# Optimization experiments

Hardware: AMD Instinct MI355X
Metric: run time of the kernel (lower is better)

## Reference

```python
import jax, jax.numpy as jnp
import numpy as np

B, N, D = 16384, 30, 128  # batch, max_neighbors, model_dim


def setup_inputs() -> dict:
    key = jax.random.key(0)
    k1, k2, k3, k4, k5 = jax.random.split(key, 5)
    rel_embeds = jax.random.normal(k1, (B, N, D), dtype=jnp.float32)
    ent_embeds = jax.random.normal(k2, (B, N, D), dtype=jnp.float32)
    mask = jax.random.randint(k3, (B, N), 0, 2).astype(jnp.bool_)  # True = masked
    # neigh_att_W: Linear(2D -> D), xavier-normal weight; neigh_att_u: Linear(D -> 1)
    std_w = float(np.sqrt(2.0 / (2 * D + D)))
    W_w = jax.random.normal(k4, (D, 2 * D), dtype=jnp.float32) * std_w
    b_w = jnp.zeros((D,), dtype=jnp.float32)
    std_u = float(np.sqrt(2.0 / (D + 1)))
    W_u = jax.random.normal(k5, (1, D), dtype=jnp.float32) * std_u
    b_u = jnp.zeros((1,), dtype=jnp.float32)
    return {"rel_embeds": rel_embeds, "ent_embeds": ent_embeds, "mask": mask,
            "W_w": W_w, "b_w": b_w, "W_u": W_u, "b_u": b_u}


def reference(rel_embeds, ent_embeds, mask, W_w, b_w, W_u, b_u):
    # concat along feature dim -> [B, N, 2D]
    concat = jnp.concatenate([rel_embeds, ent_embeds], axis=-1)
    h = jnp.tanh(jnp.einsum('bnf,df->bnd', concat, W_w) + b_w)      # [B, N, D]
    att = jnp.einsum('bnd,od->bno', h, W_u) + b_u                   # [B, N, 1]
    att = jnp.where(mask[..., None], -jnp.inf, att)
    att = jax.nn.softmax(att, axis=1)[..., 0]                       # [B, N]
    out = jnp.einsum('bn,bnd->bd', att, ent_embeds)                 # [B, D]
    return jnp.tanh(out)
```

## Files before the change

### kernel.cpp

```cpp
#include <hip/hip_runtime.h>
#include <cstdint>
#include <cstddef>


#define WAVES 4
#define BLOCK 256
#define NPAD 32
#define LDS_STRIDE 264

typedef __attribute__((ext_vector_type(8))) short short8;
typedef __attribute__((ext_vector_type(4))) float f32x4;

__device__ __forceinline__ float fast_tanh(float x) {
  float e = __expf(2.0f * x);
  return 1.0f - 2.0f / (e + 1.0f);
}

__device__ __forceinline__ void cvt_hilo(float f, unsigned short& h, unsigned short& l) {
  unsigned int bits = __float_as_uint(f);
  h = (unsigned short)(bits >> 16);
  float r = f - __uint_as_float(bits & 0xFFFF0000u);
  l = (unsigned short)(__float_as_uint(r) >> 16);
}

__global__ __launch_bounds__(BLOCK, 2) void hetrognn_kernel(
    const float* __restrict__ rel, const float* __restrict__ ent,
    const int* __restrict__ mask, const float* __restrict__ Ww,
    const float* __restrict__ bw, const float* __restrict__ Wu,
    const float* __restrict__ bu, float* __restrict__ out, int Btot) {
  __shared__ unsigned short Ahi[NPAD * LDS_STRIDE];
  __shared__ unsigned short Alo[NPAD * LDS_STRIDE];
  __shared__ float pscore[WAVES][NPAD];
  __shared__ float att[NPAD];

  const int tid = threadIdx.x;
  const int wave = tid >> 6;
  const int lane = tid & 63;
  const int l15 = lane & 15;
  const int quad = lane >> 4;

  short8 whi[2][8], wlo[2][8];
  float bwv[2], uv[2];
#pragma unroll
  for (int c = 0; c < 2; ++c) {
    const int d = wave * 32 + c * 16 + l15;
    bwv[c] = bw[d];
    uv[c] = Wu[d];
#pragma unroll
    for (int ks = 0; ks < 8; ++ks) {
      const float* wp = Ww + d * 256 + ks * 32 + quad * 8;
#pragma unroll
      for (int j = 0; j < 8; ++j) {
        unsigned short h, l;
        cvt_hilo(wp[j], h, l);
        whi[c][ks][j] = (short)h;
        wlo[c][ks][j] = (short)l;
      }
    }
  }
  const float buv = bu[0];

  for (int b = blockIdx.x; b < Btot; b += gridDim.x) {
    const float* rel_b = rel + (size_t)b * 3840;
    const float* ent_b = ent + (size_t)b * 3840;

#pragma unroll
    for (int it = 0; it < 8; ++it) {
      const int i4 = tid + it * 256;
      const int row = i4 >> 6;
      const int k4 = (i4 & 63) << 2;
      float4 v = make_float4(0.f, 0.f, 0.f, 0.f);
      if (row < 30) {
        const float* src = (k4 < 128) ? (rel_b + row * 128 + k4)
                                      : (ent_b + row * 128 + (k4 - 128));
        v = *(const float4*)src;
      }
      unsigned short h0, h1, h2, h3, l0, l1, l2, l3;
      cvt_hilo(v.x, h0, l0);
      cvt_hilo(v.y, h1, l1);
      cvt_hilo(v.z, h2, l2);
      cvt_hilo(v.w, h3, l3);
      uint2 hh, ll;
      hh.x = (unsigned int)h0 | ((unsigned int)h1 << 16);
      hh.y = (unsigned int)h2 | ((unsigned int)h3 << 16);
      ll.x = (unsigned int)l0 | ((unsigned int)l1 << 16);
      ll.y = (unsigned int)l2 | ((unsigned int)l3 << 16);
      *(uint2*)&Ahi[row * LDS_STRIDE + k4] = hh;
      *(uint2*)&Alo[row * LDS_STRIDE + k4] = ll;
    }
    __syncthreads();

#pragma unroll
    for (int mt = 0; mt < 2; ++mt) {
      f32x4 acc0 = {0.f, 0.f, 0.f, 0.f};
      f32x4 acc1 = {0.f, 0.f, 0.f, 0.f};
      const int arow = mt * 16 + l15;
      const unsigned short* abase = &Ahi[arow * LDS_STRIDE + quad * 8];
      const unsigned short* lbase = &Alo[arow * LDS_STRIDE + quad * 8];
#pragma unroll
      for (int ks = 0; ks < 8; ++ks) {
        short8 ah = *(const short8*)(abase + ks * 32);
        short8 al = *(const short8*)(lbase + ks * 32);
        acc0 = __builtin_amdgcn_mfma_f32_16x16x32_bf16(ah, whi[0][ks], acc0, 0, 0, 0);
        acc1 = __builtin_amdgcn_mfma_f32_16x16x32_bf16(ah, whi[1][ks], acc1, 0, 0, 0);
        acc0 = __builtin_amdgcn_mfma_f32_16x16x32_bf16(al, whi[0][ks], acc0, 0, 0, 0);
        acc1 = __builtin_amdgcn_mfma_f32_16x16x32_bf16(al, whi[1][ks], acc1, 0, 0, 0);
        acc0 = __builtin_amdgcn_mfma_f32_16x16x32_bf16(ah, wlo[0][ks], acc0, 0, 0, 0);
        acc1 = __builtin_amdgcn_mfma_f32_16x16x32_bf16(ah, wlo[1][ks], acc1, 0, 0, 0);
      }
      float part[4];
#pragma unroll
      for (int reg = 0; reg < 4; ++reg) {
        float h0 = fast_tanh(acc0[reg] + bwv[0]);
        float h1 = fast_tanh(acc1[reg] + bwv[1]);
        part[reg] = uv[0] * h0 + uv[1] * h1;
      }
#pragma unroll
      for (int m = 1; m < 16; m <<= 1) {
#pragma unroll
        for (int reg = 0; reg < 4; ++reg) part[reg] += __shfl_xor(part[reg], m, 64);
      }
      float v = (l15 == 0) ? part[0] : (l15 == 1) ? part[1] : (l15 == 2) ? part[2] : part[3];
      if (l15 < 4) pscore[wave][mt * 16 + quad * 4 + l15] = v;
    }
    __syncthreads();

    if (tid < 32) {
      const int n = tid;
      float raw = pscore[0][n] + pscore[1][n] + pscore[2][n] + pscore[3][n] + buv;
      const bool valid = (n < 30) && (mask[(size_t)b * 30 + n] == 0);
      float sc = valid ? raw : -INFINITY;
      float mx = sc;
#pragma unroll
      for (int m = 1; m < 32; m <<= 1) mx = fmaxf(mx, __shfl_xor(mx, m, 64));
      float e = valid ? __expf(sc - mx) : 0.f;
      float sm = e;
#pragma unroll
      for (int m = 1; m < 32; m <<= 1) sm += __shfl_xor(sm, m, 64);
      att[n] = e / sm;
    }
    __syncthreads();

    if (tid < 128) {
      const int d = tid;
      const float* ep = ent_b + d;
      float acc = 0.f;
#pragma unroll
      for (int n = 0; n < 30; ++n) acc += att[n] * ep[n * 128];
      out[(size_t)b * 128 + d] = fast_tanh(acc);
    }
    __syncthreads();
  }
}

extern "C" void kernel_launch(void* const* d_in, const int* in_sizes, int n_in,
                              void* d_out, int out_size, void* d_ws, size_t ws_size,
                              hipStream_t stream) {
  const float* rel = (const float*)d_in[0];
  const float* ent = (const float*)d_in[1];
  const int* mask = (const int*)d_in[2];
  const float* Ww = (const float*)d_in[3];
  const float* bw = (const float*)d_in[4];
  const float* Wu = (const float*)d_in[5];
  const float* bu = (const float*)d_in[6];
  float* out = (float*)d_out;
  const int Btot = in_sizes[0] / 3840;
  const int grid = 2048;
  hipLaunchKernelGGL(hetrognn_kernel, dim3(grid), dim3(BLOCK), 0, stream,
                     rel, ent, mask, Ww, bw, Wu, bu, out, Btot);
}
```

Before: 613.4 us.

## Prefetch next batch row into registers while computing current one

The embedding and mask loads for the next batch element are issued into registers before the MFMA, softmax and output phases of the current element run, so global-memory latency overlaps with compute. The final per-iteration barrier is dropped, since the existing barriers already order the shared-memory reuse. The output reduction is split into two accumulators to shorten the dependency chain. The cost is 32 extra VGPRs for the prefetch buffer, which may raise register pressure under the 2-blocks-per-CU launch bound.

```diff
diff --git a/kernel.cpp b/kernel.cpp
--- a/kernel.cpp
+++ b/kernel.cpp
@@ -16,11 +16,11 @@
   return 1.0f - 2.0f / (e + 1.0f);
 }
 
-__device__ __forceinline__ void cvt_hilo(float f, unsigned short& h, unsigned short& l) {
+__device__ __forceinline__ void cvt_hilo(float f, unsigned int& h, unsigned int& l) {
   unsigned int bits = __float_as_uint(f);
-  h = (unsigned short)(bits >> 16);
+  h = bits >> 16;
   float r = f - __uint_as_float(bits & 0xFFFF0000u);
-  l = (unsigned short)(__float_as_uint(r) >> 16);
+  l = __float_as_uint(r) >> 16;
 }
 
 __global__ __launch_bounds__(BLOCK, 2) void hetrognn_kernel(
@@ -51,7 +51,7 @@
       const float* wp = Ww + d * 256 + ks * 32 + quad * 8;
 #pragma unroll
       for (int j = 0; j < 8; ++j) {
-        unsigned short h, l;
+        unsigned int h, l;
         cvt_hilo(wp[j], h, l);
         whi[c][ks][j] = (short)h;
         wlo[c][ks][j] = (short)l;
@@ -60,33 +60,62 @@
   }
   const float buv = bu[0];
 
-  for (int b = blockIdx.x; b < Btot; b += gridDim.x) {
-    const float* rel_b = rel + (size_t)b * 3840;
-    const float* ent_b = ent + (size_t)b * 3840;
-
+  float4 v[8];
+  const int b0 = blockIdx.x;
+  {
+    const float* rb = rel + (size_t)b0 * 3840;
+    const float* eb = ent + (size_t)b0 * 3840;
 #pragma unroll
     for (int it = 0; it < 8; ++it) {
       const int i4 = tid + it * 256;
       const int row = i4 >> 6;
       const int k4 = (i4 & 63) << 2;
-      float4 v = make_float4(0.f, 0.f, 0.f, 0.f);
-      if (row < 30) {
-        const float* src = (k4 < 128) ? (rel_b + row * 128 + k4)
-                                      : (ent_b + row * 128 + (k4 - 128));
-        v = *(const float4*)src;
-      }
-      unsigned short h0, h1, h2, h3, l0, l1, l2, l3;
-      cvt_hilo(v.x, h0, l0);
-      cvt_hilo(v.y, h1, l1);
-      cvt_hilo(v.z, h2, l2);
-      cvt_hilo(v.w, h3, l3);
+      v[it] = make_float4(0.f, 0.f, 0.f, 0.f);
+      if (row < 30)
+        v[it] = *(const float4*)((k4 < 128) ? (rb + row * 128 + k4)
+                                            : (eb + row * 128 + (k4 - 128)));
+    }
+  }
+  int mcur = 1;
+  if (tid < 30) mcur = mask[(size_t)b0 * 30 + tid];
+
+  for (int b = b0; b < Btot; b += gridDim.x) {
+#pragma unroll
+    for (int it = 0; it < 8; ++it) {
+      const int i4 = tid + it * 256;
+      const int row = i4 >> 6;
+      const int k4 = (i4 & 63) << 2;
+      unsigned int h0, h1, h2, h3, l0, l1, l2, l3;
+      cvt_hilo(v[it].x, h0, l0);
+      cvt_hilo(v[it].y, h1, l1);
+      cvt_hilo(v[it].z, h2, l2);
+      cvt_hilo(v[it].w, h3, l3);
       uint2 hh, ll;
-      hh.x = (unsigned int)h0 | ((unsigned int)h1 << 16);
-      hh.y = (unsigned int)h2 | ((unsigned int)h3 << 16);
-      ll.x = (unsigned int)l0 | ((unsigned int)l1 << 16);
-      ll.y = (unsigned int)l2 | ((unsigned int)l3 << 16);
+      hh.x = h0 | (h1 << 16);
+      hh.y = h2 | (h3 << 16);
+      ll.x = l0 | (l1 << 16);
+      ll.y = l2 | (l3 << 16);
       *(uint2*)&Ahi[row * LDS_STRIDE + k4] = hh;
       *(uint2*)&Alo[row * LDS_STRIDE + k4] = ll;
+    }
+
+    const int bn = b + (int)gridDim.x;
+    int mnext = 1;
+    if (bn < Btot) {
+      const float* rb = rel + (size_t)bn * 3840;
+      const float* eb = ent + (size_t)bn * 3840;
+#pragma unroll
+      for (int it = 0; it < 8; ++it) {
+        const int i4 = tid + it * 256;
+        const int row = i4 >> 6;
+        const int k4 = (i4 & 63) << 2;
+        if (row < 30)
+          v[it] = *(const float4*)((k4 < 128) ? (rb + row * 128 + k4)
+                                              : (eb + row * 128 + (k4 - 128)));
+        else
+          v[it] = make_float4(0.f, 0.f, 0.f, 0.f);
+      }
+      if (tid < 30) mnext = mask[(size_t)bn * 30 + tid];
     }
     __syncthreads();
 
@@ -120,15 +149,15 @@
 #pragma unroll
         for (int reg = 0; reg < 4; ++reg) part[reg] += __shfl_xor(part[reg], m, 64);
       }
-      float v = (l15 == 0) ? part[0] : (l15 == 1) ? part[1] : (l15 == 2) ? part[2] : part[3];
-      if (l15 < 4) pscore[wave][mt * 16 + quad * 4 + l15] = v;
+      float pv = (l15 == 0) ? part[0] : (l15 == 1) ? part[1] : (l15 == 2) ? part[2] : part[3];
+      if (l15 < 4) pscore[wave][mt * 16 + quad * 4 + l15] = pv;
     }
     __syncthreads();
 
     if (tid < 32) {
       const int n = tid;
       float raw = pscore[0][n] + pscore[1][n] + pscore[2][n] + pscore[3][n] + buv;
-      const bool valid = (n < 30) && (mask[(size_t)b * 30 + n] == 0);
+      const bool valid = (n < 30) && (mcur == 0);
       float sc = valid ? raw : -INFINITY;
       float mx = sc;
 #pragma unroll
@@ -139,17 +168,19 @@
       for (int m = 1; m < 32; m <<= 1) sm += __shfl_xor(sm, m, 64);
       att[n] = e / sm;
     }
+    mcur = mnext;
     __syncthreads();
 
     if (tid < 128) {
-      const int d = tid;
-      const float* ep = ent_b + d;
-      float acc = 0.f;
-#pragma unroll
-      for (int n = 0; n < 30; ++n) acc += att[n] * ep[n * 128];
-      out[(size_t)b * 128 + d] = fast_tanh(acc);
-    }
-    __syncthreads();
+      const float* ep = ent + (size_t)b * 3840 + tid;
+      float a0 = 0.f, a1 = 0.f;
+#pragma unroll
+      for (int n = 0; n < 30; n += 2) {
+        a0 += att[n] * ep[n * 128];
+        a1 += att[n + 1] * ep[(n + 1) * 128];
+      }
+      out[(size_t)b * 128 + tid] = fast_tanh(a0 + a1);
+    }
   }
 }
 
```

New measurement: 665.8 us. 8.6% more time.

## Process two batch items per block iteration with DPP row reductions

Applied to the files above, without the earlier changes.

Each block iteration now handles two batch elements, filling a 64-row LDS tile and running four MFMA row tiles. Each wave therefore reuses its register-resident weights across more rows, and the per-iteration barrier and softmax overhead is spread over two items. The cross-lane sums use DPP row operations instead of shuffles. The mask load is hoisted before the staging loop, and the final weighted sum uses all 256 threads with two accumulators. LDS use doubles to about 68 KB, which may limit occupancy, and with 2048 blocks each block handles only 4 pairs, so load imbalance is possible.

```diff
diff --git a/kernel.cpp b/kernel.cpp
--- a/kernel.cpp
+++ b/kernel.cpp
@@ -5,7 +5,7 @@
 
 #define WAVES 4
 #define BLOCK 256
-#define NPAD 32
+#define ROWS 64
 #define LDS_STRIDE 264
 
 typedef __attribute__((ext_vector_type(8))) short short8;
@@ -16,11 +16,24 @@
   return 1.0f - 2.0f / (e + 1.0f);
 }
 
-__device__ __forceinline__ void cvt_hilo(float f, unsigned short& h, unsigned short& l) {
+__device__ __forceinline__ void cvt_hilo(float f, unsigned int& h, unsigned int& l) {
   unsigned int bits = __float_as_uint(f);
-  h = (unsigned short)(bits >> 16);
+  h = bits >> 16;
   float r = f - __uint_as_float(bits & 0xFFFF0000u);
-  l = (unsigned short)(__float_as_uint(r) >> 16);
+  l = __float_as_uint(r) >> 16;
+}
+
+template <int CTRL>
+__device__ __forceinline__ float dpp_add(float x) {
+  return x + __int_as_float(
+      __builtin_amdgcn_update_dpp(0, __float_as_int(x), CTRL, 0xF, 0xF, true));
+}
+__device__ __forceinline__ float row16_sum(float x) {
+  x = dpp_add<0xB1>(x);
+  x = dpp_add<0x4E>(x);
+  x = dpp_add<0x141>(x);
+  x = dpp_add<0x140>(x);
+  return x;
 }
 
 __global__ __launch_bounds__(BLOCK, 2) void hetrognn_kernel(
@@ -28,10 +41,10 @@
     const int* __restrict__ mask, const float* __restrict__ Ww,
     const float* __restrict__ bw, const float* __restrict__ Wu,
     const float* __restrict__ bu, float* __restrict__ out, int Btot) {
-  __shared__ unsigned short Ahi[NPAD * LDS_STRIDE];
-  __shared__ unsigned short Alo[NPAD * LDS_STRIDE];
-  __shared__ float pscore[WAVES][NPAD];
-  __shared__ float att[NPAD];
+  __shared__ unsigned short Ahi[ROWS * LDS_STRIDE];
+  __shared__ unsigned short Alo[ROWS * LDS_STRIDE];
+  __shared__ float pscore[WAVES][ROWS];
+  __shared__ float att[ROWS];
 
   const int tid = threadIdx.x;
   const int wave = tid >> 6;
@@ -51,7 +64,7 @@
       const float* wp = Ww + d * 256 + ks * 32 + quad * 8;
 #pragma unroll
       for (int j = 0; j < 8; ++j) {
-        unsigned short h, l;
+        unsigned int h, l;
         cvt_hilo(wp[j], h, l);
         whi[c][ks][j] = (short)h;
         wlo[c][ks][j] = (short)l;
@@ -60,38 +73,55 @@
   }
   const float buv = bu[0];
 
-  for (int b = blockIdx.x; b < Btot; b += gridDim.x) {
-    const float* rel_b = rel + (size_t)b * 3840;
-    const float* ent_b = ent + (size_t)b * 3840;
-
-#pragma unroll
-    for (int it = 0; it < 8; ++it) {
-      const int i4 = tid + it * 256;
-      const int row = i4 >> 6;
-      const int k4 = (i4 & 63) << 2;
-      float4 v = make_float4(0.f, 0.f, 0.f, 0.f);
-      if (row < 30) {
-        const float* src = (k4 < 128) ? (rel_b + row * 128 + k4)
-                                      : (ent_b + row * 128 + (k4 - 128));
-        v = *(const float4*)src;
-      }
-      unsigned short h0, h1, h2, h3, l0, l1, l2, l3;
-      cvt_hilo(v.x, h0, l0);
-      cvt_hilo(v.y, h1, l1);
-      cvt_hilo(v.z, h2, l2);
-      cvt_hilo(v.w, h3, l3);
-      uint2 hh, ll;
-      hh.x = (unsigned int)h0 | ((unsigned int)h1 << 16);
-      hh.y = (unsigned int)h2 | ((unsigned int)h3 << 16);
-      ll.x = (unsigned int)l0 | ((unsigned int)l1 << 16);
-      ll.y = (unsigned int)l2 | ((unsigned int)l3 << 16);
-      *(uint2*)&Ahi[row * LDS_STRIDE + k4] = hh;
-      *(uint2*)&Alo[row * LDS_STRIDE + k4] = ll;
-    }
-    __syncthreads();
-
-#pragma unroll
-    for (int mt = 0; mt < 2; ++mt) {
+  const int pairs = (Btot + 1) >> 1;
+  for (int p = blockIdx.x; p < pairs; p += gridDim.x) {
+    const int bA = p * 2;
+    const int bB = bA + 1;
+
+    int mreg = 1;
+    if (tid < 64) {
+      const int n = tid & 31;
+      const int bb = bA + (tid >> 5);
+      if (n < 30 && bb < Btot) mreg = mask[(size_t)bb * 30 + n];
+    }
+
+#pragma unroll
+    for (int half = 0; half < 2; ++half) {
+      const int bb = bA + half;
+      const bool bvalid = (bb < Btot);
+      const float* rb = rel + (size_t)bb * 3840;
+      const float* eb = ent + (size_t)bb * 3840;
+      const int rowbase = half * 32;
+#pragma unroll
+      for (int it = 0; it < 8; ++it) {
+        const int i4 = tid + it * 256;
+        const int row = i4 >> 6;
+        const int k4 = (i4 & 63) << 2;
+        float4 v = make_float4(0.f, 0.f, 0.f, 0.f);
+        if (bvalid && row < 30) {
+          const float* src = (k4 < 128) ? (rb + row * 128 + k4)
+                                        : (eb + row * 128 + (k4 - 128));
+          v = *(const float4*)src;
+        }
+        unsigned int h0, h1, h2, h3, l0, l1, l2, l3;
+        cvt_hilo(v.x, h0, l0);
+        cvt_hilo(v.y, h1, l1);
+        cvt_hilo(v.z, h2, l2);
+        cvt_hilo(v.w, h3, l3);
+        uint2 hh, ll;
+        hh.x = h0 | (h1 << 16);
+        hh.y = h2 | (h3 << 16);
+        ll.x = l0 | (l1 << 16);
+        ll.y = l2 | (l3 << 16);
+        *(uint2*)&Ahi[(rowbase + row) * LDS_STRIDE + k4] = hh;
+        *(uint2*)&Alo[(rowbase + row) * LDS_STRIDE + k4] = ll;
+      }
+      asm volatile("" ::: "memory");
+    }
+    __syncthreads();
+
+#pragma unroll
+    for (int mt = 0; mt < 4; ++mt) {
       f32x4 acc0 = {0.f, 0.f, 0.f, 0.f};
       f32x4 acc1 = {0.f, 0.f, 0.f, 0.f};
       const int arow = mt * 16 + l15;
@@ -116,38 +146,45 @@
         part[reg] = uv[0] * h0 + uv[1] * h1;
       }
 #pragma unroll
-      for (int m = 1; m < 16; m <<= 1) {
-#pragma unroll
-        for (int reg = 0; reg < 4; ++reg) part[reg] += __shfl_xor(part[reg], m, 64);
-      }
-      float v = (l15 == 0) ? part[0] : (l15 == 1) ? part[1] : (l15 == 2) ? part[2] : part[3];
-      if (l15 < 4) pscore[wave][mt * 16 + quad * 4 + l15] = v;
-    }
-    __syncthreads();
-
-    if (tid < 32) {
-      const int n = tid;
-      float raw = pscore[0][n] + pscore[1][n] + pscore[2][n] + pscore[3][n] + buv;
-      const bool valid = (n < 30) && (mask[(size_t)b * 30 + n] == 0);
+      for (int reg = 0; reg < 4; ++reg) part[reg] = row16_sum(part[reg]);
+      float pv = (l15 == 0) ? part[0] : (l15 == 1) ? part[1] : (l15 == 2) ? part[2] : part[3];
+      if (l15 < 4) pscore[wave][mt * 16 + quad * 4 + l15] = pv;
+    }
+    __syncthreads();
+
+    if (tid < 64) {
+      const int n = tid & 31;
+      const int base = tid & 32;
+      float raw = pscore[0][base + n] + pscore[1][base + n] +
+                  pscore[2][base + n] + pscore[3][base + n] + buv;
+      const bool valid = (n < 30) && (mreg == 0);
       float sc = valid ? raw : -INFINITY;
       float mx = sc;
 #pragma unroll
-      for (int m = 1; m < 32; m <<= 1) mx = fmaxf(mx, __shfl_xor(mx, m, 64));
+      for (int m = 1; m < 32; m <<= 1) mx = fmaxf(mx, __shfl_xor(mx, m, 32));
       float e = valid ? __expf(sc - mx) : 0.f;
       float sm = e;
 #pragma unroll
-      for (int m = 1; m < 32; m <<= 1) sm += __shfl_xor(sm, m, 64);
-      att[n] = e / sm;
-    }
-    __syncthreads();
-
-    if (tid < 128) {
-      const int d = tid;
-      const float* ep = ent_b + d;
-      float acc = 0.f;
-#pragma unroll
-      for (int n = 0; n < 30; ++n) acc += att[n] * ep[n * 128];
-      out[(size_t)b * 128 + d] = fast_tanh(acc);
+      for (int m = 1; m < 32; m <<= 1) sm += __shfl_xor(sm, m, 32);
+      att[base + n] = e / sm;
+    }
+    __syncthreads();
+
+    {
+      const int half = tid >> 7;
+      const int d = tid & 127;
+      const int bb = bA + half;
+      if (bb < Btot) {
+        const float* ep = ent + (size_t)bb * 3840 + d;
+        const float* ap = &att[half * 32];
+        float a0 = 0.f, a1 = 0.f;
+#pragma unroll
+        for (int n = 0; n < 30; n += 2) {
+          a0 += ap[n] * ep[n * 128];
+          a1 += ap[n + 1] * ep[(n + 1) * 128];
+        }
+        out[(size_t)bb * 128 + d] = fast_tanh(a0 + a1);
+      }
     }
     __syncthreads();
   }
```

Result: slower. 649.5 us (+5.9%).
